# Performance work log

Hardware: AMD Instinct MI355X
Metric: run time of the kernel (lower is better)

The kernel has to match this reference:

```python
import jax, jax.numpy as jnp
import numpy as np

DECAY = 0.8
EPS = 1e-05


def setup_inputs() -> dict:
    key = jax.random.key(0)
    k1, k2, k3 = jax.random.split(key, 3)
    b, n, d = 16, 4096, 64
    h, c = 1, 2048
    x = jax.random.normal(k1, (b, n, d), dtype=jnp.float32)
    embeddings = jax.random.normal(k2, (h, c, d), dtype=jnp.float32)
    cluster_size = jnp.ones((h, c), dtype=jnp.float32)
    embed_avg = jax.random.normal(k3, (h, c, d), dtype=jnp.float32)
    return {"x": x, "embeddings": embeddings, "cluster_size": cluster_size, "embed_avg": embed_avg}


def reference(x, embeddings, cluster_size, embed_avg):
    # x: (b, n, d); add codebook dim h=1 and flatten -> (h, N, d)
    d = x.shape[-1]
    flat = x.reshape(1, -1, d)                              # (h, N, d)
    h, C = embeddings.shape[0], embeddings.shape[1]

    # dist = -cdist(flat, embeddings)  (negative euclidean distance)
    x2 = jnp.sum(flat * flat, axis=-1, keepdims=True)       # (h, N, 1)
    e2 = jnp.sum(embeddings * embeddings, axis=-1)          # (h, C)
    xe = jnp.einsum('hnd,hcd->hnc', flat, embeddings)       # (h, N, C)
    dist = -jnp.sqrt(jnp.clip(x2 + e2[:, None, :] - 2.0 * xe, 0.0))

    # gumbel_sample with stochastic=False, straight_through=False -> hard argmax
    embed_ind = jnp.argmax(dist, axis=-1)                   # (h, N)

    # quantize: gather selected codes
    quantize = jnp.take_along_axis(embeddings, embed_ind[..., None], axis=1)  # (h, N, d)

    # EMA codebook update (scatter-based): counts and per-code feature sums
    counts = jax.vmap(lambda i: jnp.bincount(i, length=C))(embed_ind).astype(x.dtype)  # (h, C)
    embed_sum = jax.vmap(lambda f, i: jax.ops.segment_sum(f, i, num_segments=C))(flat, embed_ind)  # (h, C, d)

    new_cluster_size = cluster_size * DECAY + counts * (1.0 - DECAY)
    new_embed_avg = embed_avg * DECAY + embed_sum * (1.0 - DECAY)

    # laplace smoothing of cluster sizes, then renormalize embed_avg
    tot = jnp.sum(new_cluster_size, axis=-1, keepdims=True)
    smoothed = (new_cluster_size + EPS) / (tot + C * EPS) * tot
    new_embeddings = new_embed_avg / smoothed[..., None]

    quantize = quantize.reshape(x.shape)                    # drop h dim back to (b, n, d)
    embed_ind = embed_ind.reshape(x.shape[:-1])             # (b, n)
    return quantize, embed_ind, new_embeddings, new_cluster_size, new_embed_avg
```

## Files before the change

### kernel.cpp

```cpp
#include <hip/hip_runtime.h>

#define N_TOK 65536
#define D 64
#define C_CODES 2048
#define DECAYF 0.8f
#define OMDF 0.2f
#define EPSF 1e-5f
#define SEG 16
#define GAP_THR 0.0625f
#define TCODES 64
#define NTILES (C_CODES / TCODES)

#define OUT_QUANT 0
#define OUT_IND   (N_TOK * D)
#define OUT_EMB   (OUT_IND + N_TOK)
#define OUT_CS    (OUT_EMB + C_CODES * D)
#define OUT_EAVG  (OUT_CS + C_CODES)

typedef short s16x8 __attribute__((ext_vector_type(8)));
typedef float f32x4 __attribute__((ext_vector_type(4)));

__device__ __forceinline__ unsigned short f2bf(float f) {
    unsigned int u = __float_as_uint(f);
    return (unsigned short)((u + 0x7fffu + ((u >> 16) & 1u)) >> 16);
}
__device__ __forceinline__ float bf2f(unsigned short h) {
    return __uint_as_float(((unsigned int)h) << 16);
}
__device__ __forceinline__ unsigned long long shflx64w(unsigned long long v, int mask, int w) {
    unsigned int lo = (unsigned int)v, hi = (unsigned int)(v >> 32);
    lo = __shfl_xor(lo, mask, w);
    hi = __shfl_xor(hi, mask, w);
    return ((unsigned long long)hi << 32) | lo;
}
__device__ __forceinline__ void gload_lds16(const void* g, void* l) {
    __builtin_amdgcn_global_load_lds(
        (const __attribute__((address_space(1))) void*)g,
        (__attribute__((address_space(3))) void*)l, 16, 0, 0);
}

__global__ void eprep_kernel(const float* __restrict__ emb, short* __restrict__ ebk,
                             float* __restrict__ e2, unsigned int* __restrict__ e2p,
                             float* __restrict__ counts, float* __restrict__ embed_sum,
                             int* __restrict__ pend_n) {
    int g = blockIdx.x * blockDim.x + threadIdx.x;
    int code = g >> 3, slot = g & 7;
    int kc = slot ^ (code & 7);
    const float4* ep = (const float4*)(emb + (size_t)code * D + kc * 8);
    float4 a = ep[0], b = ep[1];
    float v[8] = {a.x, a.y, a.z, a.w, b.x, b.y, b.z, b.w};
    s16x8 h, l;
#pragma unroll
    for (int j = 0; j < 8; ++j) {
        unsigned short hb = f2bf(v[j]);
        h[j] = (short)hb;
        l[j] = (short)f2bf(v[j] - bf2f(hb));
    }
    *(s16x8*)(ebk + (size_t)code * 128 + slot * 8) = h;
    *(s16x8*)(ebk + (size_t)code * 128 + 64 + slot * 8) = l;

    float4 z = {0.f, 0.f, 0.f, 0.f};
    ((float4*)embed_sum)[g * 2] = z;
    ((float4*)embed_sum)[g * 2 + 1] = z;
    if (g < C_CODES / 4) ((float4*)counts)[g] = z;
    if (g == 0) pend_n[0] = 0;

    if (g < C_CODES) {
        const float4* er = (const float4*)(emb + (size_t)g * D);
        float s0 = 0.f, s1 = 0.f, s2 = 0.f, s3 = 0.f;
#pragma unroll
        for (int i = 0; i < D / 4; ++i) {
            float4 e = er[i];
            s0 = fmaf(e.x, e.x, s0);
            s1 = fmaf(e.y, e.y, s1);
            s2 = fmaf(e.z, e.z, s2);
            s3 = fmaf(e.w, e.w, s3);
        }
        float vv = (s0 + s1) + (s2 + s3);
        e2[g] = vv;
        unsigned short hb = f2bf(vv);
        unsigned short lb = f2bf(vv - bf2f(hb));
        e2p[g] = (unsigned int)hb | ((unsigned int)lb << 16);
    }
}

__global__ __launch_bounds__(256) void screen_kernel(
        const float* __restrict__ x, const float* __restrict__ emb,
        const short* __restrict__ ebk, const float* __restrict__ e2,
        const unsigned int* __restrict__ e2p,
        int* __restrict__ idx, float* __restrict__ out, float* __restrict__ counts,
        int* __restrict__ pend_n, unsigned int* __restrict__ pend) {
    __shared__ unsigned int e2pl[C_CODES];
    __shared__ __align__(16) char bstage[2][TCODES * 256];
    __shared__ unsigned int fin[4][32][5];

    const int tid = threadIdx.x;
    ((uint4*)e2pl)[tid] = ((const uint4*)e2p)[tid];
    ((uint4*)e2pl)[tid + 256] = ((const uint4*)e2p)[tid + 256];

    const int lane = tid & 63;
    const int wave = tid >> 6;
    const int col = lane & 15;
    const int krow = lane >> 4;

    s16x8 ah[2][2], al[2][2];
#pragma unroll
    for (int s = 0; s < 2; ++s) {
        int tok = blockIdx.x * 128 + wave * 32 + s * 16 + col;
        const float4* xp = (const float4*)(x + (size_t)tok * D + krow * 8);
        float4 f0 = xp[0], f1 = xp[1], f2 = xp[8], f3 = xp[9];
        float xv[16] = {f0.x, f0.y, f0.z, f0.w, f1.x, f1.y, f1.z, f1.w,
                        f2.x, f2.y, f2.z, f2.w, f3.x, f3.y, f3.z, f3.w};
#pragma unroll
        for (int j = 0; j < 8; ++j) {
            float v0 = -2.0f * xv[j];
            unsigned short h0 = f2bf(v0);
            ah[s][0][j] = (short)h0;
            al[s][0][j] = (short)f2bf(v0 - bf2f(h0));
            float v1 = -2.0f * xv[8 + j];
            unsigned short h1 = f2bf(v1);
            ah[s][1][j] = (short)h1;
            al[s][1][j] = (short)f2bf(v1 - bf2f(h1));
        }
    }

    s16x8 aone = {0, 0, 0, 0, 0, 0, 0, 0};
    {
        short o = (krow == 0) ? (short)0x3F80 : (short)0;
        aone[0] = o;
        aone[1] = o;
    }
    const f32x4 zero = {0.f, 0.f, 0.f, 0.f};

    float b1[2][4], b2[2][4], b3[2][4];
    unsigned int c1[2][4], c2[2][4];
#pragma unroll
    for (int s = 0; s < 2; ++s)
#pragma unroll
        for (int r = 0; r < 4; ++r) {
            b1[s][r] = __builtin_inff();
            b2[s][r] = __builtin_inff();
            b3[s][r] = __builtin_inff();
            c1[s][r] = 0u;
            c2[s][r] = 0u;
        }

    auto stage = [&](int b, int t) {
        const char* src = (const char*)ebk + (size_t)t * (TCODES * 256)
                          + wave * 4096 + lane * 16;
        char* dst = &bstage[b][wave * 4096];
        gload_lds16(src, dst);
        gload_lds16(src + 1024, dst + 1024);
        gload_lds16(src + 2048, dst + 2048);
        gload_lds16(src + 3072, dst + 3072);
    };

    auto subtile = [&](const char* lb, int t, int j) {
        const char* base = lb + (j << 12) + (col << 8);
        int off = (krow ^ (col & 7)) << 4;
        s16x8 bh0 = *(const s16x8*)(base + off);
        s16x8 bh1 = *(const s16x8*)(base + (off ^ 64));
        s16x8 bl0 = *(const s16x8*)(base + 128 + off);
        s16x8 bl1 = *(const s16x8*)(base + 128 + (off ^ 64));
        int sloc = t * 4 + j;
        unsigned int cg = (unsigned int)(sloc * 16 + col);
        unsigned int v = e2pl[sloc * 16 + col];
        v = (krow == 0) ? v : 0u;
        s16x8 be2 = {(short)(v & 0xffffu), (short)(v >> 16), 0, 0, 0, 0, 0, 0};
        f32x4 f = __builtin_amdgcn_mfma_f32_16x16x32_bf16(aone, be2, zero, 0, 0, 0);
#pragma unroll
        for (int s = 0; s < 2; ++s) {
            f32x4 acc = __builtin_amdgcn_mfma_f32_16x16x32_bf16(ah[s][1], bh1, f, 0, 0, 0);
            acc = __builtin_amdgcn_mfma_f32_16x16x32_bf16(ah[s][0], bh0, acc, 0, 0, 0);
            acc = __builtin_amdgcn_mfma_f32_16x16x32_bf16(al[s][1], bh1, acc, 0, 0, 0);
            acc = __builtin_amdgcn_mfma_f32_16x16x32_bf16(al[s][0], bh0, acc, 0, 0, 0);
            acc = __builtin_amdgcn_mfma_f32_16x16x32_bf16(ah[s][1], bl1, acc, 0, 0, 0);
            acc = __builtin_amdgcn_mfma_f32_16x16x32_bf16(ah[s][0], bl0, acc, 0, 0, 0);
#pragma unroll
            for (int r = 0; r < 4; ++r) {
                float sc = acc[r];
                bool l1 = sc < b1[s][r];
                bool l2 = sc < b2[s][r];
                b3[s][r] = __builtin_amdgcn_fmed3f(b2[s][r], b3[s][r], sc);
                b2[s][r] = __builtin_amdgcn_fmed3f(b1[s][r], b2[s][r], sc);
                unsigned int tc = l1 ? c1[s][r] : cg;
                c2[s][r] = l2 ? tc : c2[s][r];
                b1[s][r] = fminf(b1[s][r], sc);
                c1[s][r] = l1 ? cg : c1[s][r];
            }
        }
    };

    stage(0, 0);
    __syncthreads();

    for (int t = 0; t < NTILES; ++t) {
        if (t + 1 < NTILES) stage((t + 1) & 1, t + 1);
        const char* lb = bstage[t & 1];
        subtile(lb, t, 0);
        subtile(lb, t, 1);
        subtile(lb, t, 2);
        subtile(lb, t, 3);
        __syncthreads();
    }

#pragma unroll
    for (int s = 0; s < 2; ++s)
#pragma unroll
        for (int r = 0; r < 4; ++r) {
            float B1 = b1[s][r], B2 = b2[s][r], B3 = b3[s][r];
            unsigned int C1 = c1[s][r], C2 = c2[s][r];
#pragma unroll
            for (int mk = 1; mk < 16; mk <<= 1) {
                float o1 = __shfl_xor(B1, mk, 16);
                float o2 = __shfl_xor(B2, mk, 16);
                float o3 = __shfl_xor(B3, mk, 16);
                unsigned int oc1 = (unsigned int)__shfl_xor((int)C1, mk, 16);
                unsigned int oc2 = (unsigned int)__shfl_xor((int)C2, mk, 16);
                bool ta = B1 <= o1;
                float x1v = ta ? o1 : B1;
                unsigned int xc = ta ? oc1 : C1;
                float nm1 = ta ? B1 : o1;
                unsigned int nc1 = ta ? C1 : oc1;
                bool tb = B2 <= o2;
                float y1v = tb ? B2 : o2;
                unsigned int yc = tb ? C2 : oc2;
                bool tc = x1v <= y1v;
                float nm2 = tc ? x1v : y1v;
                unsigned int nc2 = tc ? xc : yc;
                float nm3 = fminf(fmaxf(x1v, y1v), fminf(B3, o3));
                B1 = nm1; C1 = nc1; B2 = nm2; C2 = nc2; B3 = nm3;
            }
            if (col == 0) {
                int tl = s * 16 + krow * 4 + r;
                fin[wave][tl][0] = __float_as_uint(B1);
                fin[wave][tl][1] = C1;
                fin[wave][tl][2] = __float_as_uint(B2);
                fin[wave][tl][3] = C2;
                fin[wave][tl][4] = __float_as_uint(B3);
            }
        }
    __syncthreads();

    if (lane < 32) {
        const unsigned int* f = fin[wave][lane];
        float m1 = __uint_as_float(f[0]);
        int cm1 = (int)f[1];
        float m2 = __uint_as_float(f[2]);
        int cm2 = (int)f[3];
        float m3 = __uint_as_float(f[4]);
        int tok = blockIdx.x * 128 + wave * 32 + lane;
        bool uniq = (m2 - m1 > GAP_THR);
        bool pairf = !uniq && (m3 - m1 > GAP_THR);
        int c = cm1;

        if (pairf) {
            int ca = cm1, cb = cm2;
            float xs[4] = {0.f, 0.f, 0.f, 0.f};
            float da[4] = {0.f, 0.f, 0.f, 0.f};
            float db[4] = {0.f, 0.f, 0.f, 0.f};
            for (int q = 0; q < 4; ++q) {
                const float4* xq = (const float4*)(x + (size_t)tok * D + q * 16);
                const float4* ea = (const float4*)(emb + (size_t)ca * D + q * 16);
                const float4* eb = (const float4*)(emb + (size_t)cb * D + q * 16);
#pragma unroll
                for (int j = 0; j < 4; ++j) {
                    float4 xv = xq[j], av = ea[j], bv = eb[j];
                    xs[0] = fmaf(xv.x, xv.x, xs[0]);
                    xs[1] = fmaf(xv.y, xv.y, xs[1]);
                    xs[2] = fmaf(xv.z, xv.z, xs[2]);
                    xs[3] = fmaf(xv.w, xv.w, xs[3]);
                    da[0] = fmaf(xv.x, av.x, da[0]);
                    da[1] = fmaf(xv.y, av.y, da[1]);
                    da[2] = fmaf(xv.z, av.z, da[2]);
                    da[3] = fmaf(xv.w, av.w, da[3]);
                    db[0] = fmaf(xv.x, bv.x, db[0]);
                    db[1] = fmaf(xv.y, bv.y, db[1]);
                    db[2] = fmaf(xv.z, bv.z, db[2]);
                    db[3] = fmaf(xv.w, bv.w, db[3]);
                }
            }
            float x2 = (xs[0] + xs[1]) + (xs[2] + xs[3]);
            float dota = (da[0] + da[1]) + (da[2] + da[3]);
            float dA = fmaxf(x2 + e2[ca] - 2.0f * dota, 0.0f);
            float dotb = (db[0] + db[1]) + (db[2] + db[3]);
            float dB = fmaxf(x2 + e2[cb] - 2.0f * dotb, 0.0f);
            unsigned long long ka =
                ((unsigned long long)__float_as_uint(dA) << 32) | (unsigned int)ca;
            unsigned long long kb =
                ((unsigned long long)__float_as_uint(dB) << 32) | (unsigned int)cb;
            c = (int)((ka < kb ? ka : kb) & 0xffffffffull);
        }

        if (uniq || pairf) {
            idx[tok] = c;
            out[OUT_IND + tok] = (float)c;
            atomicAdd(&counts[c], 1.0f);
        } else {
            int p = atomicAdd(pend_n, 1);
            pend[p] = (unsigned int)tok;
        }
    }
}

__global__ __launch_bounds__(256) void cleanup_kernel(
        const float* __restrict__ x, const float* __restrict__ emb,
        const float* __restrict__ e2, const int* __restrict__ pend_n,
        const unsigned int* __restrict__ pend,
        int* __restrict__ idx, float* __restrict__ out, float* __restrict__ counts) {
    int gw = (int)((blockIdx.x * blockDim.x + threadIdx.x) >> 6);
    int nw = (int)((gridDim.x * blockDim.x) >> 6);
    int lane = threadIdx.x & 63;
    int M = pend_n[0];
    for (int i = gw; i < M; i += nw) {
        int tn = (int)pend[i];
        float xs[4] = {0.f, 0.f, 0.f, 0.f};
        for (int q = 0; q < 4; ++q) {
            const float4* xq = (const float4*)(x + (size_t)tn * D + q * 16);
#pragma unroll
            for (int j = 0; j < 4; ++j) {
                float4 xv = xq[j];
                xs[0] = fmaf(xv.x, xv.x, xs[0]);
                xs[1] = fmaf(xv.y, xv.y, xs[1]);
                xs[2] = fmaf(xv.z, xv.z, xs[2]);
                xs[3] = fmaf(xv.w, xv.w, xs[3]);
            }
        }
        float tx2 = (xs[0] + xs[1]) + (xs[2] + xs[3]);
        unsigned long long kbest = ~0ull;
        for (int cc = lane; cc < C_CODES; cc += 64) {
            float d0 = 0.f, d1 = 0.f, d2 = 0.f, d3 = 0.f;
            for (int q = 0; q < 4; ++q) {
                const float4* xq = (const float4*)(x + (size_t)tn * D + q * 16);
                const float4* er = (const float4*)(emb + (size_t)cc * D + q * 16);
#pragma unroll
                for (int j = 0; j < 4; ++j) {
                    float4 xv = xq[j], ev = er[j];
                    d0 = fmaf(xv.x, ev.x, d0);
                    d1 = fmaf(xv.y, ev.y, d1);
                    d2 = fmaf(xv.z, ev.z, d2);
                    d3 = fmaf(xv.w, ev.w, d3);
                }
            }
            float dot = (d0 + d1) + (d2 + d3);
            float dist2 = fmaxf(tx2 + e2[cc] - 2.0f * dot, 0.0f);
            unsigned long long key =
                ((unsigned long long)__float_as_uint(dist2) << 32) | (unsigned int)cc;
            kbest = key < kbest ? key : kbest;
        }
#pragma unroll
        for (int mk = 1; mk < 64; mk <<= 1) {
            unsigned long long o = shflx64w(kbest, mk, 64);
            kbest = o < kbest ? o : kbest;
        }
        if (lane == 0) {
            int c = (int)(kbest & 0xffffffffull);
            idx[tn] = c;
            out[OUT_IND + tn] = (float)c;
            atomicAdd(&counts[c], 1.0f);
        }
    }
}

__global__ void gather_kernel(const float* __restrict__ emb,
                              const int* __restrict__ idx,
                              float* __restrict__ out) {
    int g = blockIdx.x * blockDim.x + threadIdx.x;
    int n = g >> 4;
    int j = g & 15;
    int c = idx[n];
    float4 e = ((const float4*)emb)[c * (D / 4) + j];
    ((float4*)(out + OUT_QUANT))[g] = e;
}

__global__ void prefix_ema_kernel(const float* __restrict__ counts,
                                  const float* __restrict__ cluster_size,
                                  float* __restrict__ out,
                                  float* __restrict__ smoothed,
                                  int* __restrict__ cursor) {
    __shared__ float scan[256];
    __shared__ float red[256];
    int t = threadIdx.x;
    int base = t * 8;
    float cnt[8], ncs[8];
    float csum = 0.f, nsum = 0.f;
#pragma unroll
    for (int j = 0; j < 8; ++j) {
        cnt[j] = counts[base + j];
        csum += cnt[j];
        ncs[j] = cluster_size[base + j] * DECAYF + cnt[j] * OMDF;
        nsum += ncs[j];
        out[OUT_CS + base + j] = ncs[j];
    }
    scan[t] = csum;
    red[t] = nsum;
    __syncthreads();
    for (int s = 1; s < 256; s <<= 1) {
        float v = scan[t];
        float w = (t >= s) ? scan[t - s] : 0.f;
        __syncthreads();
        scan[t] = v + w;
        __syncthreads();
    }
    for (int s = 128; s > 0; s >>= 1) {
        if (t < s) red[t] += red[t + s];
        __syncthreads();
    }
    float tot = red[0];
    float run = (t == 0) ? 0.f : scan[t - 1];
#pragma unroll
    for (int j = 0; j < 8; ++j) {
        cursor[base + j] = (int)run;
        run += cnt[j];
        smoothed[base + j] = (ncs[j] + EPSF) / (tot + (float)C_CODES * EPSF) * tot;
    }
}

__global__ void scatter_pos_kernel(const int* __restrict__ idx,
                                   int* __restrict__ cursor,
                                   unsigned int* __restrict__ sorted) {
    int n = blockIdx.x * blockDim.x + threadIdx.x;
    int c = idx[n];
    int pos = atomicAdd(&cursor[c], 1);
    sorted[pos] = ((unsigned int)c << 16) | (unsigned int)n;
}

__global__ __launch_bounds__(256) void seg_sum_kernel(
        const float* __restrict__ x, const unsigned int* __restrict__ sorted,
        float* __restrict__ embed_sum) {
    int lane = threadIdx.x & 63;
    int q = blockIdx.x * 4 + (threadIdx.x >> 6);
    int p0 = q * SEG;

    unsigned int mine = (lane < SEG) ? sorted[p0 + lane] : 0u;
    unsigned int pk[SEG];
#pragma unroll
    for (int j = 0; j < SEG; ++j) pk[j] = __shfl(mine, j, 64);

    float xv[SEG];
#pragma unroll
    for (int j = 0; j < SEG; ++j)
        xv[j] = x[(size_t)(pk[j] & 0xffffu) * D + lane];

    unsigned int run_c = 0xffffffffu;
    float sum = 0.f;
#pragma unroll
    for (int j = 0; j < SEG; ++j) {
        unsigned int c = pk[j] >> 16;
        if (c != run_c) {
            if (run_c != 0xffffffffu)
                atomicAdd(&embed_sum[(size_t)run_c * D + lane], sum);
            run_c = c;
            sum = 0.f;
        }
        sum += xv[j];
    }
    atomicAdd(&embed_sum[(size_t)run_c * D + lane], sum);
}

__global__ void ema_embed_kernel(const float* __restrict__ embed_avg,
                                 const float* __restrict__ embed_sum,
                                 const float* __restrict__ smoothed,
                                 float* __restrict__ out) {
    int g = blockIdx.x * blockDim.x + threadIdx.x;
    int c = g >> 4;
    float4 ea = ((const float4*)embed_avg)[g];
    float4 es = ((const float4*)embed_sum)[g];
    float4 na;
    na.x = ea.x * DECAYF + es.x * OMDF;
    na.y = ea.y * DECAYF + es.y * OMDF;
    na.z = ea.z * DECAYF + es.z * OMDF;
    na.w = ea.w * DECAYF + es.w * OMDF;
    ((float4*)(out + OUT_EAVG))[g] = na;
    float sm = smoothed[c];
    float4 ne;
    ne.x = na.x / sm;
    ne.y = na.y / sm;
    ne.z = na.z / sm;
    ne.w = na.w / sm;
    ((float4*)(out + OUT_EMB))[g] = ne;
}

extern "C" void kernel_launch(void* const* d_in, const int* in_sizes, int n_in,
                              void* d_out, int out_size, void* d_ws, size_t ws_size,
                              hipStream_t stream) {
    const float* x            = (const float*)d_in[0];
    const float* emb          = (const float*)d_in[1];
    const float* cluster_size = (const float*)d_in[2];
    const float* embed_avg    = (const float*)d_in[3];
    float* out = (float*)d_out;

    float* e2        = (float*)d_ws;
    unsigned int* e2p = (unsigned int*)(e2 + C_CODES);
    float* counts    = (float*)(e2p + C_CODES);
    float* smoothed  = counts + C_CODES;
    int*   cursor    = (int*)(smoothed + C_CODES);
    int*   idx       = cursor + C_CODES;
    unsigned int* sorted = (unsigned int*)(idx + N_TOK);
    int*   pend_n    = (int*)(sorted + N_TOK);
    unsigned int* pend = (unsigned int*)(pend_n + 4);
    float* embed_sum = (float*)(pend + N_TOK);
    short* ebk       = (short*)(embed_sum + C_CODES * D);

    eprep_kernel<<<(C_CODES * 8) / 256, 256, 0, stream>>>(emb, ebk, e2, e2p, counts,
                                                          embed_sum, pend_n);
    screen_kernel<<<N_TOK / 128, 256, 0, stream>>>(x, emb, ebk, e2, e2p, idx, out,
                                                   counts, pend_n, pend);
    cleanup_kernel<<<128, 256, 0, stream>>>(x, emb, e2, pend_n, pend, idx, out, counts);
    gather_kernel<<<(N_TOK * 16) / 256, 256, 0, stream>>>(emb, idx, out);
    prefix_ema_kernel<<<1, 256, 0, stream>>>(counts, cluster_size, out, smoothed, cursor);
    scatter_pos_kernel<<<N_TOK / 256, 256, 0, stream>>>(idx, cursor, sorted);
    seg_sum_kernel<<<(N_TOK / SEG) / 4, 256, 0, stream>>>(x, sorted, embed_sum);
    ema_embed_kernel<<<(C_CODES * 16) / 256, 256, 0, stream>>>(embed_avg, embed_sum,
                                                              smoothed, out);
}
```

Before: 270.9 us.

## Split codebook screening across two block halves and merge top-3 in new kernel

The screening kernel now launches a 2-D grid in which each block scans only half of the codebook (1024 codes), doubling the block count from 512 to 1024 for better occupancy and latency hiding across the GPU. Each half writes its per-token top-2 candidates and third-best distance to a workspace buffer. A new merge kernel combines the two halves, runs the pair-refinement check, and queues ambiguous tokens for the existing cleanup pass. This costs an extra kernel launch plus a workspace round-trip of about 24 bytes per token per half, and the x fragments are loaded and converted twice. It also adds bounds clamping on the pending queue.

```diff
diff --git a/kernel.cpp b/kernel.cpp
--- a/kernel.cpp
+++ b/kernel.cpp
@@ -9,7 +9,7 @@
 #define SEG 16
 #define GAP_THR 0.0625f
 #define TCODES 64
-#define NTILES (C_CODES / TCODES)
+#define HT (1024 / TCODES)
 
 #define OUT_QUANT 0
 #define OUT_IND   (N_TOK * D)
@@ -37,6 +37,24 @@
     __builtin_amdgcn_global_load_lds(
         (const __attribute__((address_space(1))) void*)g,
         (__attribute__((address_space(3))) void*)l, 16, 0, 0);
+}
+
+__device__ __forceinline__ void merge3(
+        float a1, unsigned int ca1, float a2, unsigned int ca2, float a3,
+        float b1, unsigned int cb1, float b2, unsigned int cb2, float b3,
+        float& m1, unsigned int& cm1, float& m2, unsigned int& cm2, float& m3) {
+    bool ta = a1 <= b1;
+    m1 = ta ? a1 : b1;
+    cm1 = ta ? ca1 : cb1;
+    float x1v = ta ? b1 : a1;
+    unsigned int xc = ta ? cb1 : ca1;
+    bool tb = a2 <= b2;
+    float y1v = tb ? a2 : b2;
+    unsigned int yc = tb ? ca2 : cb2;
+    bool tc = x1v <= y1v;
+    m2 = tc ? x1v : y1v;
+    cm2 = tc ? xc : yc;
+    m3 = fminf(fmaxf(x1v, y1v), fminf(a3, b3));
 }
 
 __global__ void eprep_kernel(const float* __restrict__ emb, short* __restrict__ ebk,
@@ -85,18 +103,15 @@
 }
 
 __global__ __launch_bounds__(256) void screen_kernel(
-        const float* __restrict__ x, const float* __restrict__ emb,
-        const short* __restrict__ ebk, const float* __restrict__ e2,
-        const unsigned int* __restrict__ e2p,
-        int* __restrict__ idx, float* __restrict__ out, float* __restrict__ counts,
-        int* __restrict__ pend_n, unsigned int* __restrict__ pend) {
-    __shared__ unsigned int e2pl[C_CODES];
+        const float* __restrict__ x, const short* __restrict__ ebk,
+        const unsigned int* __restrict__ e2p, uint4* __restrict__ ktop2,
+        float* __restrict__ kb3) {
+    __shared__ unsigned int e2pl[1024];
     __shared__ __align__(16) char bstage[2][TCODES * 256];
-    __shared__ unsigned int fin[4][32][5];
 
     const int tid = threadIdx.x;
-    ((uint4*)e2pl)[tid] = ((const uint4*)e2p)[tid];
-    ((uint4*)e2pl)[tid + 256] = ((const uint4*)e2p)[tid + 256];
+    const int bh = blockIdx.y;
+    ((uint4*)e2pl)[tid] = ((const uint4*)(e2p + bh * 1024))[tid];
 
     const int lane = tid & 63;
     const int wave = tid >> 6;
@@ -146,7 +161,7 @@
         }
 
     auto stage = [&](int b, int t) {
-        const char* src = (const char*)ebk + (size_t)t * (TCODES * 256)
+        const char* src = (const char*)ebk + (size_t)(bh * HT + t) * (TCODES * 256)
                           + wave * 4096 + lane * 16;
         char* dst = &bstage[b][wave * 4096];
         gload_lds16(src, dst);
@@ -163,7 +178,7 @@
         s16x8 bl0 = *(const s16x8*)(base + 128 + off);
         s16x8 bl1 = *(const s16x8*)(base + 128 + (off ^ 64));
         int sloc = t * 4 + j;
-        unsigned int cg = (unsigned int)(sloc * 16 + col);
+        unsigned int cg = (unsigned int)(bh * 1024 + sloc * 16 + col);
         unsigned int v = e2pl[sloc * 16 + col];
         v = (krow == 0) ? v : 0u;
         s16x8 be2 = {(short)(v & 0xffffu), (short)(v >> 16), 0, 0, 0, 0, 0, 0};
@@ -194,8 +209,8 @@
     stage(0, 0);
     __syncthreads();
 
-    for (int t = 0; t < NTILES; ++t) {
-        if (t + 1 < NTILES) stage((t + 1) & 1, t + 1);
+    for (int t = 0; t < HT; ++t) {
+        if (t + 1 < HT) stage((t + 1) & 1, t + 1);
         const char* lb = bstage[t & 1];
         subtile(lb, t, 0);
         subtile(lb, t, 1);
@@ -217,89 +232,89 @@
                 float o3 = __shfl_xor(B3, mk, 16);
                 unsigned int oc1 = (unsigned int)__shfl_xor((int)C1, mk, 16);
                 unsigned int oc2 = (unsigned int)__shfl_xor((int)C2, mk, 16);
-                bool ta = B1 <= o1;
-                float x1v = ta ? o1 : B1;
-                unsigned int xc = ta ? oc1 : C1;
-                float nm1 = ta ? B1 : o1;
-                unsigned int nc1 = ta ? C1 : oc1;
-                bool tb = B2 <= o2;
-                float y1v = tb ? B2 : o2;
-                unsigned int yc = tb ? C2 : oc2;
-                bool tc = x1v <= y1v;
-                float nm2 = tc ? x1v : y1v;
-                unsigned int nc2 = tc ? xc : yc;
-                float nm3 = fminf(fmaxf(x1v, y1v), fminf(B3, o3));
+                float nm1, nm2, nm3;
+                unsigned int nc1, nc2;
+                merge3(B1, C1, B2, C2, B3, o1, oc1, o2, oc2, o3,
+                       nm1, nc1, nm2, nc2, nm3);
                 B1 = nm1; C1 = nc1; B2 = nm2; C2 = nc2; B3 = nm3;
             }
             if (col == 0) {
-                int tl = s * 16 + krow * 4 + r;
-                fin[wave][tl][0] = __float_as_uint(B1);
-                fin[wave][tl][1] = C1;
-                fin[wave][tl][2] = __float_as_uint(B2);
-                fin[wave][tl][3] = C2;
-                fin[wave][tl][4] = __float_as_uint(B3);
+                int tok = blockIdx.x * 128 + wave * 32 + s * 16 + krow * 4 + r;
+                uint4 o;
+                o.x = __float_as_uint(B1);
+                o.y = C1;
+                o.z = __float_as_uint(B2);
+                o.w = C2;
+                ktop2[(size_t)tok * 2 + bh] = o;
+                kb3[(size_t)tok * 2 + bh] = B3;
             }
         }
-    __syncthreads();
-
-    if (lane < 32) {
-        const unsigned int* f = fin[wave][lane];
-        float m1 = __uint_as_float(f[0]);
-        int cm1 = (int)f[1];
-        float m2 = __uint_as_float(f[2]);
-        int cm2 = (int)f[3];
-        float m3 = __uint_as_float(f[4]);
-        int tok = blockIdx.x * 128 + wave * 32 + lane;
-        bool uniq = (m2 - m1 > GAP_THR);
-        bool pairf = !uniq && (m3 - m1 > GAP_THR);
-        int c = cm1;
-
-        if (pairf) {
-            int ca = cm1, cb = cm2;
-            float xs[4] = {0.f, 0.f, 0.f, 0.f};
-            float da[4] = {0.f, 0.f, 0.f, 0.f};
-            float db[4] = {0.f, 0.f, 0.f, 0.f};
-            for (int q = 0; q < 4; ++q) {
-                const float4* xq = (const float4*)(x + (size_t)tok * D + q * 16);
-                const float4* ea = (const float4*)(emb + (size_t)ca * D + q * 16);
-                const float4* eb = (const float4*)(emb + (size_t)cb * D + q * 16);
-#pragma unroll
-                for (int j = 0; j < 4; ++j) {
-                    float4 xv = xq[j], av = ea[j], bv = eb[j];
-                    xs[0] = fmaf(xv.x, xv.x, xs[0]);
-                    xs[1] = fmaf(xv.y, xv.y, xs[1]);
-                    xs[2] = fmaf(xv.z, xv.z, xs[2]);
-                    xs[3] = fmaf(xv.w, xv.w, xs[3]);
-                    da[0] = fmaf(xv.x, av.x, da[0]);
-                    da[1] = fmaf(xv.y, av.y, da[1]);
-                    da[2] = fmaf(xv.z, av.z, da[2]);
-                    da[3] = fmaf(xv.w, av.w, da[3]);
-                    db[0] = fmaf(xv.x, bv.x, db[0]);
-                    db[1] = fmaf(xv.y, bv.y, db[1]);
-                    db[2] = fmaf(xv.z, bv.z, db[2]);
-                    db[3] = fmaf(xv.w, bv.w, db[3]);
-                }
+}
+
+__global__ __launch_bounds__(256) void merge_kernel(
+        const float* __restrict__ x, const float* __restrict__ emb,
+        const float* __restrict__ e2, const uint4* __restrict__ ktop2,
+        const float* __restrict__ kb3,
+        int* __restrict__ idx, float* __restrict__ out, float* __restrict__ counts,
+        int* __restrict__ pend_n, unsigned int* __restrict__ pend) {
+    int n = blockIdx.x * blockDim.x + threadIdx.x;
+
+    uint4 A = ktop2[(size_t)n * 2];
+    uint4 B = ktop2[(size_t)n * 2 + 1];
+    float a3 = kb3[(size_t)n * 2], b3v = kb3[(size_t)n * 2 + 1];
+    float m1, m2, m3;
+    unsigned int cm1u, cm2u;
+    merge3(__uint_as_float(A.x), A.y, __uint_as_float(A.z), A.w, a3,
+           __uint_as_float(B.x), B.y, __uint_as_float(B.z), B.w, b3v,
+           m1, cm1u, m2, cm2u, m3);
+
+    int c = (int)cm1u;
+    bool uniq = (m2 - m1 > GAP_THR);
+    bool pairf = !uniq && (m3 - m1 > GAP_THR);
+
+    if (pairf) {
+        int ca = c, cb = (int)cm2u;
+        float xs[4] = {0.f, 0.f, 0.f, 0.f};
+        float da[4] = {0.f, 0.f, 0.f, 0.f};
+        float db[4] = {0.f, 0.f, 0.f, 0.f};
+        for (int q = 0; q < 4; ++q) {
+            const float4* xq = (const float4*)(x + (size_t)n * D + q * 16);
+            const float4* ea = (const float4*)(emb + (size_t)ca * D + q * 16);
+            const float4* eb = (const float4*)(emb + (size_t)cb * D + q * 16);
+#pragma unroll
+            for (int j = 0; j < 4; ++j) {
+                float4 xv = xq[j], av = ea[j], bv = eb[j];
+                xs[0] = fmaf(xv.x, xv.x, xs[0]);
+                xs[1] = fmaf(xv.y, xv.y, xs[1]);
+                xs[2] = fmaf(xv.z, xv.z, xs[2]);
+                xs[3] = fmaf(xv.w, xv.w, xs[3]);
+                da[0] = fmaf(xv.x, av.x, da[0]);
+                da[1] = fmaf(xv.y, av.y, da[1]);
+                da[2] = fmaf(xv.z, av.z, da[2]);
+                da[3] = fmaf(xv.w, av.w, da[3]);
+                db[0] = fmaf(xv.x, bv.x, db[0]);
+                db[1] = fmaf(xv.y, bv.y, db[1]);
+                db[2] = fmaf(xv.z, bv.z, db[2]);
+                db[3] = fmaf(xv.w, bv.w, db[3]);
             }
-            float x2 = (xs[0] + xs[1]) + (xs[2] + xs[3]);
-            float dota = (da[0] + da[1]) + (da[2] + da[3]);
-            float dA = fmaxf(x2 + e2[ca] - 2.0f * dota, 0.0f);
-            float dotb = (db[0] + db[1]) + (db[2] + db[3]);
-            float dB = fmaxf(x2 + e2[cb] - 2.0f * dotb, 0.0f);
-            unsigned long long ka =
-                ((unsigned long long)__float_as_uint(dA) << 32) | (unsigned int)ca;
-            unsigned long long kb =
-                ((unsigned long long)__float_as_uint(dB) << 32) | (unsigned int)cb;
-            c = (int)((ka < kb ? ka : kb) & 0xffffffffull);
-        }
-
-        if (uniq || pairf) {
-            idx[tok] = c;
-            out[OUT_IND + tok] = (float)c;
-            atomicAdd(&counts[c], 1.0f);
-        } else {
-            int p = atomicAdd(pend_n, 1);
-            pend[p] = (unsigned int)tok;
-        }
+        }
+        float x2 = (xs[0] + xs[1]) + (xs[2] + xs[3]);
+        float dota = (da[0] + da[1]) + (da[2] + da[3]);
+        float dA = fmaxf(x2 + e2[ca] - 2.0f * dota, 0.0f);
+        float dotb = (db[0] + db[1]) + (db[2] + db[3]);
+        float dB = fmaxf(x2 + e2[cb] - 2.0f * dotb, 0.0f);
+        unsigned long long ka = ((unsigned long long)__float_as_uint(dA) << 32) | (unsigned int)ca;
+        unsigned long long kb = ((unsigned long long)__float_as_uint(dB) << 32) | (unsigned int)cb;
+        c = (int)((ka < kb ? ka : kb) & 0xffffffffull);
+    }
+
+    if (uniq || pairf) {
+        idx[n] = c;
+        out[OUT_IND + n] = (float)c;
+        atomicAdd(&counts[c], 1.0f);
+    } else {
+        int p = atomicAdd(pend_n, 1);
+        if (p >= 0 && p < N_TOK) pend[p] = (unsigned int)n;
     }
 }
 
@@ -312,8 +327,9 @@
     int nw = (int)((gridDim.x * blockDim.x) >> 6);
     int lane = threadIdx.x & 63;
     int M = pend_n[0];
+    M = (M < 0) ? 0 : ((M > N_TOK) ? N_TOK : M);
     for (int i = gw; i < M; i += nw) {
-        int tn = (int)pend[i];
+        int tn = (int)(pend[i] & 0xffffu);
         float xs[4] = {0.f, 0.f, 0.f, 0.f};
         for (int q = 0; q < 4; ++q) {
             const float4* xq = (const float4*)(x + (size_t)tn * D + q * 16);
@@ -499,13 +515,16 @@
     unsigned int* sorted = (unsigned int*)(idx + N_TOK);
     int*   pend_n    = (int*)(sorted + N_TOK);
     unsigned int* pend = (unsigned int*)(pend_n + 4);
-    float* embed_sum = (float*)(pend + N_TOK);
+    uint4* ktop2     = (uint4*)(pend + N_TOK);
+    float* kb3       = (float*)(ktop2 + (size_t)N_TOK * 2);
+    float* embed_sum = kb3 + (size_t)N_TOK * 2;
     short* ebk       = (short*)(embed_sum + C_CODES * D);
 
     eprep_kernel<<<(C_CODES * 8) / 256, 256, 0, stream>>>(emb, ebk, e2, e2p, counts,
                                                           embed_sum, pend_n);
-    screen_kernel<<<N_TOK / 128, 256, 0, stream>>>(x, emb, ebk, e2, e2p, idx, out,
-                                                   counts, pend_n, pend);
+    screen_kernel<<<dim3(N_TOK / 128, 2), 256, 0, stream>>>(x, ebk, e2p, ktop2, kb3);
+    merge_kernel<<<N_TOK / 256, 256, 0, stream>>>(x, emb, e2, ktop2, kb3, idx, out,
+                                                  counts, pend_n, pend);
     cleanup_kernel<<<128, 256, 0, stream>>>(x, emb, e2, pend_n, pend, idx, out, counts);
     gather_kernel<<<(N_TOK * 16) / 256, 256, 0, stream>>>(emb, idx, out);
     prefix_ema_kernel<<<1, 256, 0, stream>>>(counts, cluster_size, out, smoothed, cursor);
```

Result: slower. 279.8 us (+3.3%).
